# Kernel tuning notes

Measured on AMD Instinct MI355X. Metric: run time of the kernel, lower is better.

Reference implementation:

```python
import jax, jax.numpy as jnp
import numpy as np

B, L, E, O, K = 32, 1024, 512, 512, 4


def setup_inputs() -> dict:
    key = jax.random.key(0)
    k1, k2, k3, k4, k5, k6 = jax.random.split(key, 6)
    s = 1.0 / np.sqrt(E)
    return {
        "joint_embedding": jax.random.normal(k1, (B, L, E), dtype=jnp.float32),
        "delta_embedding": jax.random.normal(k2, (B, L, L, K), dtype=jnp.float32) * 0.1,
        "Wq": jax.random.normal(k3, (E, O), dtype=jnp.float32) * s,
        "Wk": jax.random.normal(k4, (E, O), dtype=jnp.float32) * s,
        "Wv": jax.random.normal(k5, (E, O), dtype=jnp.float32) * s,
        "traj_length": jax.random.randint(k6, (B,), 1, L + 1, dtype=jnp.int32),
    }


def reference(joint_embedding, delta_embedding, Wq, Wk, Wv, traj_length):
    # delta bias: [B, L, L, K] -> [B, L, L]
    delta = jnp.sum(delta_embedding, axis=-1)

    # mask[i, :t, :t] = 1 where t = traj_length[i], built vectorized
    pos = jnp.arange(L)
    valid = pos[None, :] < traj_length[:, None]            # [B, L]
    mask = (valid[:, :, None] & valid[:, None, :]).astype(jnp.float32)  # [B, L, L]

    q = jnp.einsum("ble,eo->blo", joint_embedding, Wq)
    k = jnp.einsum("ble,eo->blo", joint_embedding, Wk)
    v = jnp.einsum("ble,eo->blo", joint_embedding, Wv)

    scores = jnp.einsum("bqo,bko->bqk", q, k) + delta     # [B, L, L]
    attn = jax.nn.softmax(scores, axis=-1) * mask          # post-softmax mask
    return jnp.einsum("bqk,bko->bqo", attn, v)             # [B, L, O]
```

## Files before the change

kernel.cpp:

```cpp
#include <hip/hip_runtime.h>
#include <hip/hip_bf16.h>

#define Bn 32
#define Ln 1024
#define En 512
#define On 512

typedef __attribute__((ext_vector_type(8))) short bf16x8;
typedef __attribute__((ext_vector_type(4))) float f32x4;

__device__ __forceinline__ ushort f2bf(float x) {
    __hip_bfloat16 h = __float2bfloat16(x);
    return *reinterpret_cast<ushort*>(&h);
}
__device__ __forceinline__ float bf2f(ushort u) {
    __hip_bfloat16 h;
    *reinterpret_cast<ushort*>(&h) = u;
    return __bfloat162float(h);
}

__device__ __forceinline__ f32x4 mfma_bf16(bf16x8 a, bf16x8 b, f32x4 c) {
    return __builtin_amdgcn_mfma_f32_16x16x32_bf16(a, b, c, 0, 0, 0);
}

__device__ __forceinline__ void stage(ushort* dst, const ushort* src, size_t rstride) {
    const int tid = threadIdx.x;
#pragma unroll
    for (int cc = 0; cc < 2; ++cc) {
        const int c = tid + cc * 256;
        const ushort* g = src + (size_t)(c >> 2) * rstride + (c & 3) * 8;
        ushort* l = dst + ((size_t)(tid >> 6) * 64 + cc * 256) * 8;
        __builtin_amdgcn_global_load_lds(
            (const __attribute__((address_space(1))) unsigned int*)g,
            (__attribute__((address_space(3))) unsigned int*)l, 16, 0, 0);
    }
}

template <bool SPLIT>
__device__ __forceinline__ void nt_core_pipe(const ushort* __restrict__ Ah,
                                             const ushort* __restrict__ Al,
                                             const ushort* __restrict__ Bh,
                                             const ushort* __restrict__ Bl,
                                             size_t astr, size_t bstr, int Kd,
                                             f32x4 (&acc)[4][4]) {
    constexpr int NTL = SPLIT ? 4 : 2;
    constexpr int LOADS = SPLIT ? 8 : 4;
    __shared__ ushort lds[2][NTL * 4096];

    const int tid = threadIdx.x;
    const int lane = tid & 63, wave = tid >> 6;
    const int wr = (wave >> 1) * 64, wc = (wave & 1) * 64;
    const int ln = lane & 15, kb = (lane >> 4) * 8;
    const int NT = Kd >> 5;

    auto stage_all = [&](int kt, int slot) {
        const int k0 = kt * 32;
        stage(&lds[slot][0], Ah + k0, astr);
        stage(&lds[slot][4096], Bh + k0, bstr);
        if constexpr (SPLIT) {
            stage(&lds[slot][8192], Al + k0, astr);
            stage(&lds[slot][12288], Bl + k0, bstr);
        }
    };

    stage_all(0, 0);
    stage_all(1, 1);
    asm volatile("s_waitcnt vmcnt(%0)" ::"i"(LOADS) : "memory");
    __builtin_amdgcn_sched_barrier(0);
    __builtin_amdgcn_s_barrier();

    for (int t = 0; t < NT; ++t) {
        __builtin_amdgcn_sched_barrier(0);
        const int cur = t & 1;
        const ushort* sAh = &lds[cur][0];
        const ushort* sBh = &lds[cur][4096];

        bf16x8 bh[4], bl[4];
#pragma unroll
        for (int n = 0; n < 4; ++n) {
            bh[n] = *(const bf16x8*)&sBh[(size_t)(wc + n * 16 + ln) * 32 + kb];
            if constexpr (SPLIT)
                bl[n] = *(const bf16x8*)&lds[cur][12288 + (size_t)(wc + n * 16 + ln) * 32 + kb];
        }
#pragma unroll
        for (int m = 0; m < 4; ++m) {
            bf16x8 ah = *(const bf16x8*)&sAh[(size_t)(wr + m * 16 + ln) * 32 + kb];
            if constexpr (SPLIT) {
                bf16x8 al = *(const bf16x8*)&lds[cur][8192 + (size_t)(wr + m * 16 + ln) * 32 + kb];
#pragma unroll
                for (int n = 0; n < 4; ++n) {
                    acc[m][n] = mfma_bf16(ah, bh[n], acc[m][n]);
                    acc[m][n] = mfma_bf16(ah, bl[n], acc[m][n]);
                    acc[m][n] = mfma_bf16(al, bh[n], acc[m][n]);
                }
            } else {
#pragma unroll
                for (int n = 0; n < 4; ++n) acc[m][n] = mfma_bf16(ah, bh[n], acc[m][n]);
            }
        }

        asm volatile("s_waitcnt lgkmcnt(0)" ::: "memory");
        __builtin_amdgcn_sched_barrier(0);
        __builtin_amdgcn_s_barrier();

        if (t + 2 < NT) {
            stage_all(t + 2, cur);
            asm volatile("s_waitcnt vmcnt(%0)" ::"i"(LOADS) : "memory");
            __builtin_amdgcn_sched_barrier(0);
            __builtin_amdgcn_s_barrier();
        } else if (t + 1 < NT) {
            asm volatile("s_waitcnt vmcnt(0)" ::: "memory");
            __builtin_amdgcn_sched_barrier(0);
            __builtin_amdgcn_s_barrier();
        }
    }
    asm volatile("s_waitcnt vmcnt(0)" ::: "memory");
}

__global__ __launch_bounds__(256) void compute_m(const float* __restrict__ Wq,
                                                 const float* __restrict__ Wk,
                                                 ushort* __restrict__ Mthi,
                                                 ushort* __restrict__ Mtlo) {
    __shared__ float As[16][65], Bs[16][65];
    const int tid = threadIdx.x;
    const int row0 = blockIdx.y * 64;
    const int col0 = blockIdx.x * 64;
    const int tx = tid & 15, ty = tid >> 4;
    const int ar = tid >> 2, ac = (tid & 3) * 4;

    float acc[4][4] = {};
    for (int k0 = 0; k0 < On; k0 += 16) {
        float4 av = *(const float4*)&Wk[(size_t)(row0 + ar) * On + k0 + ac];
        As[ac + 0][ar] = av.x;
        As[ac + 1][ar] = av.y;
        As[ac + 2][ar] = av.z;
        As[ac + 3][ar] = av.w;
        float4 bv = *(const float4*)&Wq[(size_t)(col0 + ar) * On + k0 + ac];
        Bs[ac + 0][ar] = bv.x;
        Bs[ac + 1][ar] = bv.y;
        Bs[ac + 2][ar] = bv.z;
        Bs[ac + 3][ar] = bv.w;
        __syncthreads();
#pragma unroll
        for (int kk = 0; kk < 16; ++kk) {
            float a[4], b[4];
#pragma unroll
            for (int x = 0; x < 4; ++x) {
                a[x] = As[kk][ty * 4 + x];
                b[x] = Bs[kk][tx * 4 + x];
            }
#pragma unroll
            for (int ii = 0; ii < 4; ++ii)
#pragma unroll
                for (int jj = 0; jj < 4; ++jj) acc[ii][jj] = fmaf(a[ii], b[jj], acc[ii][jj]);
        }
        __syncthreads();
    }

#pragma unroll
    for (int ii = 0; ii < 4; ++ii)
#pragma unroll
        for (int jj = 0; jj < 4; ++jj) {
            const int i = row0 + ty * 4 + ii;
            const int j = col0 + tx * 4 + jj;
            const float f = acc[ii][jj];
            const ushort h = f2bf(f);
            Mthi[(size_t)i * En + j] = h;
            Mtlo[(size_t)i * En + j] = f2bf(f - bf2f(h));
        }
}

__global__ __launch_bounds__(256) void convert_wv(const float* __restrict__ Wv,
                                                  ushort* __restrict__ wvhi) {
    __shared__ float tile[32][33];
    const int n0 = blockIdx.x * 32, k0 = blockIdx.y * 32;
    const int tid = threadIdx.x;
    const int r = tid >> 3, c4 = (tid & 7) * 4;
    float4 wv = *(const float4*)&Wv[(size_t)(k0 + r) * On + n0 + c4];
    tile[r][c4 + 0] = wv.x;
    tile[r][c4 + 1] = wv.y;
    tile[r][c4 + 2] = wv.z;
    tile[r][c4 + 3] = wv.w;
    __syncthreads();
    ushort4 hs;
    ushort* hp = &hs.x;
#pragma unroll
    for (int jj = 0; jj < 4; ++jj) hp[jj] = f2bf(tile[c4 + jj][r]);
    *(ushort4*)&wvhi[(size_t)(n0 + r) * En + k0 + c4] = hs;
}

__global__ __launch_bounds__(256) void convert_x(const float* __restrict__ X,
                                                 ushort* __restrict__ Xhi,
                                                 ushort* __restrict__ Xlo) {
    const int g = blockIdx.x * 256 + threadIdx.x;
    const int row = g >> 6;
    const int k0 = (g & 63) * 8;
    const float* xp = X + (size_t)row * En + k0;
    float4 x0 = *(const float4*)xp;
    float4 x1 = *(const float4*)(xp + 4);
    float xs[8] = {x0.x, x0.y, x0.z, x0.w, x1.x, x1.y, x1.z, x1.w};
    bf16x8 hi, lo;
#pragma unroll
    for (int j = 0; j < 8; ++j) {
        ushort h = f2bf(xs[j]);
        hi[j] = (short)h;
        lo[j] = (short)f2bf(xs[j] - bf2f(h));
    }
    *(bf16x8*)(Xhi + (size_t)row * En + k0) = hi;
    *(bf16x8*)(Xlo + (size_t)row * En + k0) = lo;
}

__global__ __launch_bounds__(256) void gemm_y(const ushort* __restrict__ Xhi,
                                              const ushort* __restrict__ Xlo,
                                              const ushort* __restrict__ Mthi,
                                              const ushort* __restrict__ Mtlo,
                                              const int* __restrict__ traj,
                                              ushort* __restrict__ Yhi,
                                              ushort* __restrict__ Ylo) {
    const int n = blockIdx.x;
    const int xcd = n & 7;
    const int c = n >> 3;
    const int b = xcd + 8 * (c >> 5);
    const int rem = c & 31;
    const int rp = rem >> 2;
    const int x = rem & 3;
    if (rp * 128 >= traj[b]) return;
    const int row0 = b * Ln + rp * 128;
    const int col0 = x * 128;

    f32x4 acc[4][4] = {};
    nt_core_pipe<true>(Xhi + (size_t)row0 * En, Xlo + (size_t)row0 * En,
                       Mthi + (size_t)col0 * En, Mtlo + (size_t)col0 * En, En, En, En, acc);

    const int tid = threadIdx.x;
    const int lane = tid & 63, wave = tid >> 6;
    const int wr = (wave >> 1) * 64, wc = (wave & 1) * 64;
    const int ln = lane & 15;

#pragma unroll
    for (int m = 0; m < 4; ++m)
#pragma unroll
        for (int nn = 0; nn < 4; ++nn)
#pragma unroll
            for (int rr = 0; rr < 4; ++rr) {
                const int gi = row0 + wr + m * 16 + (lane >> 4) * 4 + rr;
                const int gj = col0 + wc + nn * 16 + ln;
                const float v = acc[m][nn][rr];
                const ushort h = f2bf(v);
                const size_t idx = (size_t)gi * En + gj;
                Yhi[idx] = h;
                Ylo[idx] = f2bf(v - bf2f(h));
            }
}

__global__ __launch_bounds__(256) void gemm_v(const ushort* __restrict__ Xhi,
                                              const ushort* __restrict__ wvhi,
                                              const int* __restrict__ traj,
                                              ushort* __restrict__ vt) {
    const int n = blockIdx.x;
    const int xcd = n & 7;
    const int c = n >> 3;
    const int b = xcd + 8 * (c >> 5);
    const int rem = c & 31;
    const int rp = rem >> 2;
    const int x = rem & 3;
    if (rp * 128 >= traj[b]) return;
    const int row0 = b * Ln + rp * 128;
    const int col0 = x * 128;

    f32x4 acc[4][4] = {};
    nt_core_pipe<false>(Xhi + (size_t)row0 * En, nullptr, wvhi + (size_t)col0 * En, nullptr, En,
                        En, En, acc);

    const int tid = threadIdx.x;
    const int lane = tid & 63, wave = tid >> 6;
    const int wr = (wave >> 1) * 64, wc = (wave & 1) * 64;
    const int ln = lane & 15;

    const int lbase = rp * 128;
#pragma unroll
    for (int m = 0; m < 4; ++m)
#pragma unroll
        for (int nn = 0; nn < 4; ++nn) {
            const int gj = col0 + wc + nn * 16 + ln;
            const int l0 = lbase + wr + m * 16 + (lane >> 4) * 4;
            ushort4 u;
            u.x = f2bf(acc[m][nn][0]);
            u.y = f2bf(acc[m][nn][1]);
            u.z = f2bf(acc[m][nn][2]);
            u.w = f2bf(acc[m][nn][3]);
            *(ushort4*)(vt + ((size_t)b * On + gj) * Ln + l0) = u;
        }
}

__global__ __launch_bounds__(256) void gemm_scores(const ushort* __restrict__ Yhi,
                                                   const ushort* __restrict__ Ylo,
                                                   const ushort* __restrict__ Xhi,
                                                   const ushort* __restrict__ Xlo,
                                                   const float* __restrict__ delta,
                                                   const int* __restrict__ traj,
                                                   float* __restrict__ S) {
    const int n = blockIdx.x;
    const int xcd = n & 7;
    const int c = n >> 3;
    const int b = (c / 64) * 8 + xcd;
    const int xy = c % 64;
    const int col0 = (xy & 7) * 128;
    const int row0 = (xy >> 3) * 128;
    if (row0 >= traj[b]) return;

    const size_t abase = ((size_t)b * Ln + row0) * En;
    const size_t bbase = ((size_t)b * Ln + col0) * En;

    f32x4 acc[4][4] = {};
    nt_core_pipe<true>(Yhi + abase, Ylo + abase, Xhi + bbase, Xlo + bbase, En, En, En, acc);

    const int tid = threadIdx.x;
    const int lane = tid & 63, wave = tid >> 6;
    const int wr = (wave >> 1) * 64, wc = (wave & 1) * 64;
    const int ln = lane & 15;

#pragma unroll
    for (int m = 0; m < 4; ++m)
#pragma unroll
        for (int nn = 0; nn < 4; ++nn)
#pragma unroll
            for (int rr = 0; rr < 4; ++rr) {
                const int gi = row0 + wr + m * 16 + (lane >> 4) * 4 + rr;
                const int gj = col0 + wc + nn * 16 + ln;
                const float4 dv = *(const float4*)(delta + (((size_t)b * Ln + gi) * Ln + gj) * 4);
                S[((size_t)b * Ln + gi) * Ln + gj] = acc[m][nn][rr] + ((dv.x + dv.y) + (dv.z + dv.w));
            }
}

__global__ __launch_bounds__(256) void softmax_kernel(float* __restrict__ S,
                                                      const int* __restrict__ traj) {
    const int n = blockIdx.x;
    const int xcd = n & 7;
    const int idx = n >> 3;
    const int b = xcd + 8 * (idx >> 10);
    const int i = idx & (Ln - 1);
    const int t = traj[b];
    if (i >= ((t + 127) & ~127)) return;

    float* Srow = S + ((size_t)b * Ln + i) * Ln;
    ushort* Prow = (ushort*)Srow;
    const int tid = threadIdx.x;
    const int j0 = tid * 4;

    if (i >= t) {
        ushort4 z = {0, 0, 0, 0};
        *(ushort4*)&Prow[j0] = z;
        return;
    }

    float4 v = *(const float4*)&Srow[j0];
    __shared__ float red[4];

    float m = fmaxf(fmaxf(v.x, v.y), fmaxf(v.z, v.w));
#pragma unroll
    for (int off = 32; off >= 1; off >>= 1) m = fmaxf(m, __shfl_xor(m, off));
    if ((tid & 63) == 0) red[tid >> 6] = m;
    __syncthreads();
    m = fmaxf(fmaxf(red[0], red[1]), fmaxf(red[2], red[3]));
    __syncthreads();

    float e0 = __expf(v.x - m), e1 = __expf(v.y - m), e2 = __expf(v.z - m), e3 = __expf(v.w - m);
    float s = (e0 + e1) + (e2 + e3);
#pragma unroll
    for (int off = 32; off >= 1; off >>= 1) s += __shfl_xor(s, off);
    if ((tid & 63) == 0) red[tid >> 6] = s;
    __syncthreads();
    s = (red[0] + red[1]) + (red[2] + red[3]);
    const float inv = 1.0f / s;

    ushort4 o;
    o.x = (j0 + 0 < t) ? f2bf(e0 * inv) : (ushort)0;
    o.y = (j0 + 1 < t) ? f2bf(e1 * inv) : (ushort)0;
    o.z = (j0 + 2 < t) ? f2bf(e2 * inv) : (ushort)0;
    o.w = (j0 + 3 < t) ? f2bf(e3 * inv) : (ushort)0;
    *(ushort4*)&Prow[j0] = o;
}

__global__ __launch_bounds__(256) void gemm_pv(const ushort* __restrict__ P,
                                               const ushort* __restrict__ vt,
                                               const int* __restrict__ traj,
                                               float* __restrict__ out) {
    const int n = blockIdx.x;
    const int xcd = n & 7;
    const int c = n >> 3;
    const int b = (c / 32) * 8 + xcd;
    const int xy = c % 32;
    const int col0 = (xy & 3) * 128;
    const int row0 = (xy >> 2) * 128;
    const int t = traj[b];

    const int tid = threadIdx.x;

    if (row0 >= t) {
        const float4 z = make_float4(0.f, 0.f, 0.f, 0.f);
        for (int i = tid; i < 128 * 32; i += 256) {
            const int r = i >> 5, c4 = (i & 31) * 4;
            *(float4*)&out[((size_t)b * Ln + row0 + r) * On + col0 + c4] = z;
        }
        return;
    }

    const int Kd = ((t + 31) >> 5) << 5;

    f32x4 acc[4][4] = {};
    nt_core_pipe<false>(P + ((size_t)b * Ln + row0) * 2048, nullptr,
                        vt + ((size_t)b * On + col0) * Ln, nullptr, 2048, Ln, Kd, acc);

    const int lane = tid & 63, wave = tid >> 6;
    const int wr = (wave >> 1) * 64, wc = (wave & 1) * 64;
    const int ln = lane & 15;

#pragma unroll
    for (int m = 0; m < 4; ++m)
#pragma unroll
        for (int nn = 0; nn < 4; ++nn)
#pragma unroll
            for (int rr = 0; rr < 4; ++rr) {
                const int gi = row0 + wr + m * 16 + (lane >> 4) * 4 + rr;
                const int gj = col0 + wc + nn * 16 + ln;
                const float val = (gi < t) ? acc[m][nn][rr] : 0.f;
                out[((size_t)b * Ln + gi) * On + gj] = val;
            }
}

extern "C" void kernel_launch(void* const* d_in, const int* in_sizes, int n_in,
                              void* d_out, int out_size, void* d_ws, size_t ws_size,
                              hipStream_t stream) {
    const float* X = (const float*)d_in[0];
    const float* delta = (const float*)d_in[1];
    const float* Wq = (const float*)d_in[2];
    const float* Wk = (const float*)d_in[3];
    const float* Wv = (const float*)d_in[4];
    const int* traj = (const int*)d_in[5];
    float* out = (float*)d_out;

    const size_t NE = (size_t)Bn * Ln * On;
    ushort* Mthi = (ushort*)d_ws;
    ushort* Mtlo = Mthi + (size_t)En * En;
    ushort* wvhi = Mtlo + (size_t)En * En;
    ushort* Xhi = wvhi + (size_t)En * En;
    ushort* Xlo = Xhi + NE;
    ushort* Yhi = Xlo + NE;
    ushort* Ylo = Yhi + NE;
    ushort* vt = Ylo + NE;
    float* S = (float*)(vt + NE);

    compute_m<<<dim3(En / 64, En / 64), 256, 0, stream>>>(Wq, Wk, Mthi, Mtlo);
    convert_wv<<<dim3(On / 32, En / 32), 256, 0, stream>>>(Wv, wvhi);
    convert_x<<<dim3((Bn * Ln * 64) / 256), 256, 0, stream>>>(X, Xhi, Xlo);
    gemm_y<<<dim3(1024), 256, 0, stream>>>(Xhi, Xlo, Mthi, Mtlo, traj, Yhi, Ylo);
    gemm_v<<<dim3(1024), 256, 0, stream>>>(Xhi, wvhi, traj, vt);
    gemm_scores<<<dim3(2048), 256, 0, stream>>>(Yhi, Ylo, Xhi, Xlo, delta, traj, S);
    softmax_kernel<<<dim3(Bn * Ln), 256, 0, stream>>>(S, traj);
    gemm_pv<<<dim3(1024), 256, 0, stream>>>((const ushort*)S, vt, traj, out);
}
```

Measured before the change: 373.9 us.

## Enlarge scores GEMM tile to 256x256 with direct-to-LDS double-buffered loads

Replaces the 128x128 scores GEMM with a 256x256-tile kernel of 512 threads. Each wave holds 8x4 accumulators, and hi/lo operand tiles are staged straight into LDS through global_load_lds with two-slot double buffering and explicit waitcnt barriers. The aim is more operand reuse per byte loaded and overlap of loads with the split-bf16 MFMA work. The costs are coarser early-exit granularity for short trajectories (256-row blocks), 128 accumulator registers per thread and a 128KB LDS footprint, which may limit occupancy. Only 512 blocks are launched, and the delta-bias epilogue still dominates memory traffic.

```diff
diff --git a/kernel.cpp b/kernel.cpp
--- a/kernel.cpp
+++ b/kernel.cpp
@@ -293,43 +293,108 @@
         }
 }
 
-__global__ __launch_bounds__(256) void gemm_scores(const ushort* __restrict__ Yhi,
-                                                   const ushort* __restrict__ Ylo,
-                                                   const ushort* __restrict__ Xhi,
-                                                   const ushort* __restrict__ Xlo,
-                                                   const float* __restrict__ delta,
-                                                   const int* __restrict__ traj,
-                                                   float* __restrict__ S) {
+__global__ __launch_bounds__(512, 2) void gemm_scores256(
+    const ushort* __restrict__ Yhi, const ushort* __restrict__ Ylo,
+    const ushort* __restrict__ Xhi, const ushort* __restrict__ Xlo,
+    const float* __restrict__ delta, const int* __restrict__ traj,
+    float* __restrict__ S) {
+    __shared__ ushort lds[2][4][8192];
     const int n = blockIdx.x;
     const int xcd = n & 7;
     const int c = n >> 3;
-    const int b = (c / 64) * 8 + xcd;
-    const int xy = c % 64;
-    const int col0 = (xy & 7) * 128;
-    const int row0 = (xy >> 3) * 128;
+    const int b = xcd + 8 * (c >> 4);
+    const int rem = c & 15;
+    const int rp = rem >> 2, cp = rem & 3;
+    const int row0 = rp * 256, col0 = cp * 256;
     if (row0 >= traj[b]) return;
 
-    const size_t abase = ((size_t)b * Ln + row0) * En;
-    const size_t bbase = ((size_t)b * Ln + col0) * En;
-
-    f32x4 acc[4][4] = {};
-    nt_core_pipe<true>(Yhi + abase, Ylo + abase, Xhi + bbase, Xlo + bbase, En, En, En, acc);
-
     const int tid = threadIdx.x;
     const int lane = tid & 63, wave = tid >> 6;
-    const int wr = (wave >> 1) * 64, wc = (wave & 1) * 64;
-    const int ln = lane & 15;
-
-#pragma unroll
-    for (int m = 0; m < 4; ++m)
+    const int wm = wave >> 2, wn = wave & 3;
+    const int ln = lane & 15, q4 = lane >> 4, kb = q4 * 8;
+
+    const ushort* Ah = Yhi + ((size_t)b * Ln + row0) * En;
+    const ushort* Al = Ylo + ((size_t)b * Ln + row0) * En;
+    const ushort* Bh = Xhi + ((size_t)b * Ln + col0) * En;
+    const ushort* Bl = Xlo + ((size_t)b * Ln + col0) * En;
+
+    auto stage512 = [&](ushort* dst, const ushort* src) {
+#pragma unroll
+        for (int cc = 0; cc < 2; ++cc) {
+            const int ch = tid + cc * 512;
+            const ushort* g = src + (size_t)(ch >> 2) * En + (ch & 3) * 8;
+            ushort* l = dst + ((size_t)(cc * 512 + (tid >> 6) * 64)) * 8;
+            __builtin_amdgcn_global_load_lds(
+                (const __attribute__((address_space(1))) unsigned int*)g,
+                (__attribute__((address_space(3))) unsigned int*)l, 16, 0, 0);
+        }
+    };
+    auto stage_all = [&](int kt, int slot) {
+        const int k0 = kt * 32;
+        stage512(lds[slot][0], Ah + k0);
+        stage512(lds[slot][1], Bh + k0);
+        stage512(lds[slot][2], Al + k0);
+        stage512(lds[slot][3], Bl + k0);
+    };
+
+    f32x4 acc[8][4] = {};
+
+    stage_all(0, 0);
+    stage_all(1, 1);
+    asm volatile("s_waitcnt vmcnt(8)" ::: "memory");
+    __builtin_amdgcn_sched_barrier(0);
+    __builtin_amdgcn_s_barrier();
+
+    for (int ts = 0; ts < 16; ++ts) {
+        __builtin_amdgcn_sched_barrier(0);
+        const int cur = ts & 1;
+        bf16x8 bh[4], bl[4];
+#pragma unroll
+        for (int nn = 0; nn < 4; ++nn) {
+            const size_t bo = (size_t)(wn * 64 + nn * 16 + ln) * 32 + kb;
+            bh[nn] = *(const bf16x8*)&lds[cur][1][bo];
+            bl[nn] = *(const bf16x8*)&lds[cur][3][bo];
+        }
+#pragma unroll
+        for (int m = 0; m < 8; ++m) {
+            const size_t ao = (size_t)(wm * 128 + m * 16 + ln) * 32 + kb;
+            bf16x8 ah = *(const bf16x8*)&lds[cur][0][ao];
+            bf16x8 al = *(const bf16x8*)&lds[cur][2][ao];
+#pragma unroll
+            for (int nn = 0; nn < 4; ++nn) {
+                acc[m][nn] = mfma_bf16(ah, bh[nn], acc[m][nn]);
+                acc[m][nn] = mfma_bf16(ah, bl[nn], acc[m][nn]);
+                acc[m][nn] = mfma_bf16(al, bh[nn], acc[m][nn]);
+            }
+        }
+        asm volatile("s_waitcnt lgkmcnt(0)" ::: "memory");
+        __builtin_amdgcn_sched_barrier(0);
+        __builtin_amdgcn_s_barrier();
+
+        if (ts + 2 < 16) {
+            stage_all(ts + 2, cur);
+            asm volatile("s_waitcnt vmcnt(8)" ::: "memory");
+            __builtin_amdgcn_sched_barrier(0);
+            __builtin_amdgcn_s_barrier();
+        } else if (ts + 1 < 16) {
+            asm volatile("s_waitcnt vmcnt(0)" ::: "memory");
+            __builtin_amdgcn_sched_barrier(0);
+            __builtin_amdgcn_s_barrier();
+        }
+    }
+    asm volatile("s_waitcnt vmcnt(0)" ::: "memory");
+
+#pragma unroll
+    for (int m = 0; m < 8; ++m)
 #pragma unroll
         for (int nn = 0; nn < 4; ++nn)
 #pragma unroll
             for (int rr = 0; rr < 4; ++rr) {
-                const int gi = row0 + wr + m * 16 + (lane >> 4) * 4 + rr;
-                const int gj = col0 + wc + nn * 16 + ln;
+                const int gi = row0 + wm * 128 + m * 16 + q4 * 4 + rr;
+                const int gj = col0 + wn * 64 + nn * 16 + ln;
                 const float4 dv = *(const float4*)(delta + (((size_t)b * Ln + gi) * Ln + gj) * 4);
-                S[((size_t)b * Ln + gi) * Ln + gj] = acc[m][nn][rr] + ((dv.x + dv.y) + (dv.z + dv.w));
+                S[((size_t)b * Ln + gi) * Ln + gj] =
+                    acc[m][nn][rr] + ((dv.x + dv.y) + (dv.z + dv.w));
             }
 }
 
@@ -456,7 +521,7 @@
     convert_x<<<dim3((Bn * Ln * 64) / 256), 256, 0, stream>>>(X, Xhi, Xlo);
     gemm_y<<<dim3(1024), 256, 0, stream>>>(Xhi, Xlo, Mthi, Mtlo, traj, Yhi, Ylo);
     gemm_v<<<dim3(1024), 256, 0, stream>>>(Xhi, wvhi, traj, vt);
-    gemm_scores<<<dim3(2048), 256, 0, stream>>>(Yhi, Ylo, Xhi, Xlo, delta, traj, S);
+    gemm_scores256<<<dim3(512), 512, 0, stream>>>(Yhi, Ylo, Xhi, Xlo, delta, traj, S);
     softmax_kernel<<<dim3(Bn * Ln), 256, 0, stream>>>(S, traj);
     gemm_pv<<<dim3(1024), 256, 0, stream>>>((const ushort*)S, vt, traj, out);
 }
```

After: 401.8 us. 7.5% more time.
